# Kernel optimization log

Hardware: AMD Instinct MI355X
Metric: run time of the kernel (lower is better)

## Reference

```python
import jax, jax.numpy as jnp
import numpy as np

C = 60                 # channels
WINDOW_SIZES = [4, 8, 12]
SHIFTS = 4
BN_EPS = 1e-5


def setup_inputs() -> dict:
    key = jax.random.key(0)
    ks = jax.random.split(key, 4)
    s = 0.05
    return {
        "x": jax.random.normal(ks[0], (8, C, 288, 288), dtype=jnp.float32),
        # project_inp: Conv2d(C, 2C, k=1) + BatchNorm2d(2C) (inference form)
        "W_in": jax.random.normal(ks[1], (2 * C, C), dtype=jnp.float32) * s,
        "b_in": jnp.zeros((2 * C,), dtype=jnp.float32),
        "bn_gamma": jnp.ones((2 * C,), dtype=jnp.float32),
        "bn_beta": jnp.zeros((2 * C,), dtype=jnp.float32),
        "bn_mean": jax.random.normal(ks[2], (2 * C,), dtype=jnp.float32) * s,
        "bn_var": jnp.ones((2 * C,), dtype=jnp.float32),
        # project_out: Conv2d(C, C, k=1)
        "W_out": jax.random.normal(ks[3], (C, C), dtype=jnp.float32) * s,
        "b_out": jnp.zeros((C,), dtype=jnp.float32),
    }


def _window_self_attn(x_, wsize, shift):
    """One GMSA branch: roll -> window partition -> QQ^T softmax V -> merge -> unroll.
    x_ : [b, 2c, H, W] where first c channels are q, last c are v."""
    b, c2, H, W = x_.shape
    c = c2 // 2
    if shift > 0:
        x_ = jnp.roll(x_, shift=(-(wsize // 2), -(wsize // 2)), axis=(2, 3))
    nh, nw = H // wsize, W // wsize
    # 'b (qv c) (h dh) (w dw) -> qv (b h w) (dh dw) c'
    xw = x_.reshape(b, 2, c, nh, wsize, nw, wsize)
    xw = xw.transpose(1, 0, 3, 5, 4, 6, 2).reshape(2, b * nh * nw, wsize * wsize, c)
    q, v = xw[0], xw[1]                      # [n, p, c] with p = wsize*wsize
    atn = jax.nn.softmax(jnp.einsum("npc,nqc->npq", q, q), axis=-1)
    y = jnp.einsum("npq,nqc->npc", atn, v)
    # '(b h w) (dh dw) c -> b c (h dh) (w dw)'
    y = y.reshape(b, nh, nw, wsize, wsize, c).transpose(0, 5, 1, 3, 2, 4)
    y = y.reshape(b, c, H, W)
    if shift > 0:
        y = jnp.roll(y, shift=(wsize // 2, wsize // 2), axis=(2, 3))
    return y, atn


def reference(x, W_in, b_in, bn_gamma, bn_beta, bn_mean, bn_var, W_out, b_out):
    # 1x1 conv = channel matmul, then inference BatchNorm
    xp = jnp.einsum("oc,bchw->bohw", W_in, x) + b_in[None, :, None, None]
    inv = bn_gamma / jnp.sqrt(bn_var + BN_EPS)
    xp = xp * inv[None, :, None, None] + (bn_beta - bn_mean * inv)[None, :, None, None]
    split = 2 * C // 3  # = 40 per branch (q,v interleaved as 2x20)
    ys, atns = [], []
    off = 0
    for ws in WINDOW_SIZES:
        y_, a_ = _window_self_attn(xp[:, off:off + split], ws, SHIFTS)
        off += split
        ys.append(y_)
        atns.append(a_)
    y = jnp.concatenate(ys, axis=1)  # [b, C, H, W]
    y = jnp.einsum("oc,bchw->bohw", W_out, y) + b_out[None, :, None, None]
    return (y, atns[0], atns[1], atns[2])
```

## Files before the change

### kernel.cpp

```cpp
#include <hip/hip_runtime.h>


constexpr int HW = 288 * 288;
constexpr long long ATN0_OFF = 39813120LL;
constexpr long long ATN1_OFF = ATN0_OFF + 41472LL * 256;
constexpr long long ATN2_OFF = ATN1_OFF + 10368LL * 4096;

constexpr size_t YB_OFF = 0;
constexpr size_t WP_OFF = 79626240;
constexpr size_t BP_OFF = WP_OFF + 28800;
constexpr size_t XP_OFF = BP_OFF + 512;

typedef __attribute__((ext_vector_type(8))) short     bf16x8;
typedef __attribute__((ext_vector_type(4))) short     bf16x4;
typedef __attribute__((ext_vector_type(4))) float     f32x4;
typedef __attribute__((ext_vector_type(4))) unsigned  u32x4;
typedef __attribute__((ext_vector_type(2))) unsigned  u32x2;

__device__ __forceinline__ unsigned bfrnd(float f) {
    unsigned u = __float_as_uint(f);
    return (u + 0x7fffu + ((u >> 16) & 1u)) >> 16;
}
__device__ __forceinline__ unsigned bfpack(float a, float b) { return bfrnd(a) | (bfrnd(b) << 16); }

#if defined(__has_builtin)
#if __has_builtin(__builtin_amdgcn_mfma_f32_16x16x16bf16_1k)
#define HAVE_MFMA16 1
#endif
#endif

__device__ __forceinline__ f32x4 mfma16(bf16x4 a, bf16x4 b, f32x4 c) {
#ifdef HAVE_MFMA16
    return __builtin_amdgcn_mfma_f32_16x16x16bf16_1k(a, b, c, 0, 0, 0);
#else
    f32x4 d;
    asm("v_mfma_f32_16x16x16_bf16 %0, %1, %2, %3" : "=v"(d) : "v"(a), "v"(b), "v"(c));
    return d;
#endif
}

__device__ __forceinline__ f32x4 mfma32(bf16x8 a, bf16x8 b, f32x4 c) {
    return __builtin_amdgcn_mfma_f32_16x16x32_bf16(a, b, c, 0, 0, 0);
}

__global__ void prep_kernel(const float* __restrict__ W_in, const float* __restrict__ b_in,
                            const float* __restrict__ gamma, const float* __restrict__ beta,
                            const float* __restrict__ mean, const float* __restrict__ var,
                            float* __restrict__ Wp, float* __restrict__ bp) {
    int o = threadIdx.x;
    if (o < 120) {
        float inv = gamma[o] / sqrtf(var[o] + 1e-5f);
        for (int c = 0; c < 60; ++c) Wp[o * 60 + c] = W_in[o * 60 + c] * inv;
        bp[o] = b_in[o] * inv + beta[o] - mean[o] * inv;
    } else if (o < 128) {
        bp[o] = 0.f;
    }
}

__global__ __launch_bounds__(256, 3) void proj_in_kernel(const float* __restrict__ x,
                                                         const float* __restrict__ Wp,
                                                         const float* __restrict__ bp,
                                                         unsigned short* __restrict__ xp) {
    __shared__ __align__(16) unsigned short wq[128 * 64];
    __shared__ __align__(16) unsigned short ys[128 * 120];

    const int tid = threadIdx.x;
    const long long pixel0 = (long long)blockIdx.x * 128;
    const int b   = (int)(pixel0 / HW);
    const int hw0 = (int)(pixel0 % HW);

    for (int i = tid; i < 8192; i += 256) {
        const int row = i >> 6, ch = i & 63;
        wq[i] = (row < 120 && ch < 60) ? (unsigned short)bfrnd(Wp[row * 60 + ch]) : (unsigned short)0;
    }

    const int wave = tid >> 6, lane = tid & 63, lo = lane & 15, g = lane >> 4;

    u32x4 xlo[2], xhi[2];
    #pragma unroll
    for (int mt2 = 0; mt2 < 2; ++mt2) {
        const int row = (wave * 2 + mt2) * 16 + lo;
        const float* xb = x + (long long)b * 60 * HW + hw0 + row;
        unsigned short tl[8], th[8];
        #pragma unroll
        for (int e = 0; e < 8; ++e) {
            const int cl = g * 8 + e;
            tl[e] = (unsigned short)bfrnd(xb[(long long)cl * HW]);
            const int ch = 32 + g * 8 + e;
            th[e] = (ch < 60) ? (unsigned short)bfrnd(xb[(long long)ch * HW]) : (unsigned short)0;
        }
        xlo[mt2] = *reinterpret_cast<const u32x4*>(tl);
        xhi[mt2] = *reinterpret_cast<const u32x4*>(th);
    }
    __syncthreads();

    #pragma unroll
    for (int n = 0; n < 8; ++n) {
        u32x4 wfl = *reinterpret_cast<const u32x4*>(&wq[(n * 16 + lo) * 64 + g * 8]);
        u32x4 wfh = *reinterpret_cast<const u32x4*>(&wq[(n * 16 + lo) * 64 + 32 + g * 8]);
        const int oc0 = n * 16 + 4 * g;
        const f32x4 bpv = *reinterpret_cast<const f32x4*>(&bp[oc0]);
        #pragma unroll
        for (int mt2 = 0; mt2 < 2; ++mt2) {
            f32x4 z = {0.f, 0.f, 0.f, 0.f};
            f32x4 acc = mfma32(*reinterpret_cast<bf16x8*>(&wfl),
                               *reinterpret_cast<bf16x8*>(&xlo[mt2]), z);
            acc = mfma32(*reinterpret_cast<bf16x8*>(&wfh),
                         *reinterpret_cast<bf16x8*>(&xhi[mt2]), acc);
            if (oc0 < 120) {
                const int pixel = (wave * 2 + mt2) * 16 + lo;
                u32x2 t;
                t.x = bfpack(acc[0] + bpv[0], acc[1] + bpv[1]);
                t.y = bfpack(acc[2] + bpv[2], acc[3] + bpv[3]);
                *reinterpret_cast<u32x2*>(&ys[pixel * 120 + oc0]) = t;
            }
        }
    }
    __syncthreads();

    for (int i = tid; i < 3 * 1280; i += 256) {
        const int br = i / 1280, j = i - br * 1280, p = j / 10, c = j - p * 10;
        const u32x2 v = *reinterpret_cast<const u32x2*>(&ys[p * 120 + br * 40 + c * 4]);
        reinterpret_cast<u32x2*>(xp + ((long long)(b * 3 + br) * HW + hw0) * 40)[p * 10 + c] = v;
    }
}

template <int WS, int NWIN, int BLOCK, int WPW, int BRANCH, int MINW>
__launch_bounds__(BLOCK, MINW)
__global__ void branch_kernel(const unsigned short* __restrict__ xp,
                              unsigned short* __restrict__ ybuf,
                              float* __restrict__ atn) {
    constexpr int P    = WS * WS;
    constexpr int RT   = P / 16;
    constexpr int SH   = WS / 2;
    constexpr int NWND = 288 / WS;
    constexpr int RSTR = 56;
    constexpr int WAVES = BLOCK / 64;
    constexpr int WINS_PER_WAVE = (NWIN * WPW) / WAVES;

    __shared__ __align__(16) unsigned short qv[NWIN * P * RSTR];
    __shared__ __align__(16) unsigned short ys[NWIN * P * 20];

    const int tid = threadIdx.x;
    const int w0 = blockIdx.x * NWIN;

    for (int idx = tid; idx < NWIN * P * 5; idx += BLOCK) {
        const int wl  = idx / (P * 5);
        const int rem = idx - wl * (P * 5);
        const int pix = rem / 5;
        const int ck  = rem - pix * 5;
        const int w   = w0 + wl;
        const int b   = w / (NWND * NWND);
        const int r2  = w - b * (NWND * NWND);
        const int wi  = r2 / NWND;
        const int wj  = r2 - wi * NWND;
        const int gh  = (wi * WS + pix / WS + SH) % 288;
        const int gw  = (wj * WS + pix % WS + SH) % 288;
        const u32x4 d = *reinterpret_cast<const u32x4*>(
            xp + ((long long)(b * 3 + BRANCH) * HW + gh * 288 + gw) * 40 + ck * 8);
        *reinterpret_cast<u32x4*>(&qv[(wl * P + pix) * RSTR + ck * 8]) = d;
    }
    __syncthreads();

    const int wave = tid >> 6;
    const int lane = tid & 63;
    const int lo   = lane & 15;
    const int g    = lane >> 4;

    for (int wk = 0; wk < WINS_PER_WAVE; ++wk) {
        const int wl   = (WPW == 1) ? (wave * WINS_PER_WAVE + wk) : (wave >> 1);
        const int half = (WPW == 1) ? 0 : (wave & 1);
        const int w    = w0 + wl;
        const unsigned short* wbase = qv + wl * P * RSTR;

        bf16x8 F[RT];
        #pragma unroll
        for (int t = 0; t < RT; ++t) {
            u32x4 u = *reinterpret_cast<const u32x4*>(&wbase[(16 * t + lo) * RSTR + g * 8]);
            if (g == 2) { u.z = 0; u.w = 0; }
            if (g == 3) { u.x = 0; u.y = 0; u.z = 0; u.w = 0; }
            F[t] = *reinterpret_cast<bf16x8*>(&u);
        }

        bf16x4 VB[RT][2];
        #pragma unroll
        for (int i = 0; i < RT; ++i) {
            #pragma unroll
            for (int ct = 0; ct < 2; ++ct) {
                const int c = ct * 16 + lo;
                bf16x4 vv;
                #pragma unroll
                for (int jj = 0; jj < 4; ++jj) {
                    const int row = 16 * i + 4 * g + jj;
                    vv[jj] = (c < 20) ? (short)wbase[row * RSTR + 20 + c] : (short)0;
                }
                VB[i][ct] = vv;
            }
        }

        const int jstart = (WPW == 1) ? 0 : (half * ((RT + 1) / 2));
        const int jend   = (WPW == 1) ? RT : ((half == 0) ? ((RT + 1) / 2) : RT);
        for (int j = jstart; j < jend; ++j) {
            f32x4 S[RT];
            #pragma unroll
            for (int i = 0; i < RT; ++i) {
                f32x4 z = {0.f, 0.f, 0.f, 0.f};
                S[i] = mfma32(F[i], F[j], z);
            }

            float m0 = S[0][0], m1 = S[0][1], m2 = S[0][2], m3 = S[0][3];
            #pragma unroll
            for (int i = 1; i < RT; ++i) {
                m0 = fmaxf(m0, S[i][0]); m1 = fmaxf(m1, S[i][1]);
                m2 = fmaxf(m2, S[i][2]); m3 = fmaxf(m3, S[i][3]);
            }
            float m = fmaxf(fmaxf(m0, m1), fmaxf(m2, m3));
            m = fmaxf(m, __shfl_xor(m, 16));
            m = fmaxf(m, __shfl_xor(m, 32));

            float s0 = 0.f, s1 = 0.f, s2 = 0.f, s3 = 0.f;
            #pragma unroll
            for (int i = 0; i < RT; ++i) {
                float e0 = __expf(S[i][0] - m); S[i][0] = e0; s0 += e0;
                float e1 = __expf(S[i][1] - m); S[i][1] = e1; s1 += e1;
                float e2 = __expf(S[i][2] - m); S[i][2] = e2; s2 += e2;
                float e3 = __expf(S[i][3] - m); S[i][3] = e3; s3 += e3;
            }
            float sum = (s0 + s1) + (s2 + s3);
            sum += __shfl_xor(sum, 16);
            sum += __shfl_xor(sum, 32);
            const float inv = 1.0f / sum;
            #pragma unroll
            for (int i = 0; i < RT; ++i) {
                S[i][0] *= inv; S[i][1] *= inv; S[i][2] *= inv; S[i][3] *= inv;
            }

            float* arow = atn + ((long long)w * P + 16 * j + lo) * P + 4 * g;
            #pragma unroll
            for (int i = 0; i < RT; ++i)
                __builtin_nontemporal_store(S[i], reinterpret_cast<f32x4*>(arow + 16 * i));

            f32x4 Y0 = {0.f, 0.f, 0.f, 0.f};
            f32x4 Y1 = {0.f, 0.f, 0.f, 0.f};
            #pragma unroll
            for (int i = 0; i < RT; ++i) {
                u32x2 t2;
                t2.x = bfpack(S[i][0], S[i][1]);
                t2.y = bfpack(S[i][2], S[i][3]);
                bf16x4 pa = *reinterpret_cast<bf16x4*>(&t2);
                Y0 = mfma16(pa, VB[i][0], Y0);
                Y1 = mfma16(pa, VB[i][1], Y1);
            }

            unsigned short* ywp = ys + (wl * P + 16 * j + 4 * g) * 20;
            #pragma unroll
            for (int r = 0; r < 4; ++r) ywp[r * 20 + lo] = (unsigned short)bfrnd(Y0[r]);
            if (lo < 4) {
                #pragma unroll
                for (int r = 0; r < 4; ++r) ywp[r * 20 + 16 + lo] = (unsigned short)bfrnd(Y1[r]);
            }
        }
    }
    __syncthreads();

    for (int i = tid; i < NWIN * P * 5; i += BLOCK) {
        const int wl   = i / (P * 5);
        const int rem  = i - wl * (P * 5);
        const int pixr = rem / 5;
        const int c    = rem - pixr * 5;
        const int w2   = w0 + wl;
        const int b2   = w2 / (NWND * NWND);
        const int r2   = w2 - b2 * (NWND * NWND);
        const int wi2  = r2 / NWND;
        const int wj2  = r2 - wi2 * NWND;
        const int oh   = (wi2 * WS + pixr / WS + SH) % 288;
        const int ow   = (wj2 * WS + pixr % WS + SH) % 288;
        const u32x2 v = *reinterpret_cast<const u32x2*>(&ys[(wl * P + pixr) * 20 + c * 4]);
        *reinterpret_cast<u32x2*>(
            ybuf + ((long long)(b2 * 3 + BRANCH) * HW + oh * 288 + ow) * 20 + c * 4) = v;
    }
}

__global__ __launch_bounds__(256, 4) void proj_out_kernel(const unsigned short* __restrict__ ybuf,
                                                          const float* __restrict__ W_out,
                                                          const float* __restrict__ bout,
                                                          float* __restrict__ out) {
    __shared__ __align__(16) unsigned short yh[128 * 72];
    __shared__ __align__(16) unsigned short wq[64 * 64];

    const int tid = threadIdx.x;
    const long long pixel0 = (long long)blockIdx.x * 128;
    const int b   = (int)(pixel0 / HW);
    const int hw0 = (int)(pixel0 % HW);

    for (int i = tid; i < 4096; i += 256) {
        const int row = i >> 6, ch = i & 63;
        wq[i] = (row < 60 && ch < 60) ? (unsigned short)bfrnd(W_out[row * 60 + ch]) : (unsigned short)0;
    }

    for (int i = tid; i < 1920; i += 256) {
        const int br = i / 640, j = i - br * 640, p = j / 5, c = j - p * 5;
        const u32x2 v = reinterpret_cast<const u32x2*>(
            ybuf + ((long long)(b * 3 + br) * HW + hw0) * 20)[j];
        *reinterpret_cast<u32x2*>(&yh[p * 72 + br * 20 + c * 4]) = v;
    }
    {
        const int p = tid >> 1, hh = tid & 1;
        u32x2 zz; zz.x = 0; zz.y = 0;
        *reinterpret_cast<u32x2*>(&yh[p * 72 + 60 + hh * 4]) = zz;
    }
    __syncthreads();

    const int wave = tid >> 6, lane = tid & 63, lo = lane & 15, g = lane >> 4;

    u32x4 alo[2], ahi[2];
    #pragma unroll
    for (int mt2 = 0; mt2 < 2; ++mt2) {
        const int row = (wave * 2 + mt2) * 16 + lo;
        alo[mt2] = *reinterpret_cast<const u32x4*>(&yh[row * 72 + g * 8]);
        ahi[mt2] = *reinterpret_cast<const u32x4*>(&yh[row * 72 + 32 + g * 8]);
    }

    #pragma unroll
    for (int n = 0; n < 4; ++n) {
        u32x4 wfl = *reinterpret_cast<const u32x4*>(&wq[(n * 16 + lo) * 64 + g * 8]);
        u32x4 wfh = *reinterpret_cast<const u32x4*>(&wq[(n * 16 + lo) * 64 + 32 + g * 8]);
        const int oc = n * 16 + lo;
        const float bo = (oc < 60) ? bout[oc] : 0.f;
        #pragma unroll
        for (int mt2 = 0; mt2 < 2; ++mt2) {
            f32x4 z = {0.f, 0.f, 0.f, 0.f};
            f32x4 acc = mfma32(*reinterpret_cast<bf16x8*>(&alo[mt2]),
                               *reinterpret_cast<bf16x8*>(&wfl), z);
            acc = mfma32(*reinterpret_cast<bf16x8*>(&ahi[mt2]),
                         *reinterpret_cast<bf16x8*>(&wfh), acc);
            if (oc < 60) {
                const int px = (wave * 2 + mt2) * 16 + 4 * g;
                f32x4 v;
                v[0] = acc[0] + bo; v[1] = acc[1] + bo;
                v[2] = acc[2] + bo; v[3] = acc[3] + bo;
                __builtin_nontemporal_store(v, reinterpret_cast<f32x4*>(
                    &out[((long long)b * 60 + oc) * HW + hw0 + px]));
            }
        }
    }
}

extern "C" void kernel_launch(void* const* d_in, const int* in_sizes, int n_in,
                              void* d_out, int out_size, void* d_ws, size_t ws_size,
                              hipStream_t stream) {
    const float* x     = (const float*)d_in[0];
    const float* W_in  = (const float*)d_in[1];
    const float* b_in  = (const float*)d_in[2];
    const float* gamma = (const float*)d_in[3];
    const float* beta  = (const float*)d_in[4];
    const float* mean  = (const float*)d_in[5];
    const float* var   = (const float*)d_in[6];
    const float* Wout  = (const float*)d_in[7];
    const float* bout  = (const float*)d_in[8];
    float* out = (float*)d_out;

    char* wsb = (char*)d_ws;
    unsigned short* ybuf = (unsigned short*)(wsb + YB_OFF);
    float*          Wp   = (float*)(wsb + WP_OFF);
    float*          bp   = (float*)(wsb + BP_OFF);
    unsigned short* xp   = (unsigned short*)(wsb + XP_OFF);

    prep_kernel<<<1, 128, 0, stream>>>(W_in, b_in, gamma, beta, mean, var, Wp, bp);
    proj_in_kernel<<<5184, 256, 0, stream>>>(x, Wp, bp, xp);

    branch_kernel<4,  8, 128, 1, 0, 4><<<5184, 128, 0, stream>>>(xp, ybuf, out + ATN0_OFF);
    branch_kernel<8,  2, 128, 1, 1, 4><<<5184, 128, 0, stream>>>(xp, ybuf, out + ATN1_OFF);
    branch_kernel<12, 1, 128, 2, 2, 3><<<4608, 128, 0, stream>>>(xp, ybuf, out + ATN2_OFF);

    proj_out_kernel<<<5184, 256, 0, stream>>>(ybuf, Wout, bout, out);
}
```

Baseline: 441.0 us.

## Merge three window-attention branch kernels into one interleaved launch

Replaces the three separate per-branch attention launches with a single kernel whose blocks dispatch to one of three templated bodies by block index, interleaving branches round-robin and giving the leftover branch-0/1 blocks the tail. Shared memory is unified into one buffer sized for the largest branch. The goal is to remove launch gaps and tail effects between the branch kernels and let branches with different costs overlap on the GPU. In exchange, all branches now share one register/launch-bounds setting (min 3 waves per EU) and the larger shared allocation, which may reduce occupancy for the small-window branches.

Result: slower. 452.5 us (+2.6%).

```diff
diff --git a/kernel.cpp b/kernel.cpp
--- a/kernel.cpp
+++ b/kernel.cpp
@@ -125,11 +125,11 @@
     }
 }
 
-template <int WS, int NWIN, int BLOCK, int WPW, int BRANCH, int MINW>
-__launch_bounds__(BLOCK, MINW)
-__global__ void branch_kernel(const unsigned short* __restrict__ xp,
-                              unsigned short* __restrict__ ybuf,
-                              float* __restrict__ atn) {
+template <int WS, int NWIN, int BLOCK, int WPW, int BRANCH>
+__device__ __forceinline__ void branch_body(char* smem,
+                                            const unsigned short* __restrict__ xp,
+                                            unsigned short* __restrict__ ybuf,
+                                            float* __restrict__ atn, int blk) {
     constexpr int P    = WS * WS;
     constexpr int RT   = P / 16;
     constexpr int SH   = WS / 2;
@@ -138,11 +138,11 @@
     constexpr int WAVES = BLOCK / 64;
     constexpr int WINS_PER_WAVE = (NWIN * WPW) / WAVES;
 
-    __shared__ __align__(16) unsigned short qv[NWIN * P * RSTR];
-    __shared__ __align__(16) unsigned short ys[NWIN * P * 20];
+    unsigned short* qv = reinterpret_cast<unsigned short*>(smem);
+    unsigned short* ys = reinterpret_cast<unsigned short*>(smem) + NWIN * P * RSTR;
 
     const int tid = threadIdx.x;
-    const int w0 = blockIdx.x * NWIN;
+    const int w0 = blk * NWIN;
 
     for (int idx = tid; idx < NWIN * P * 5; idx += BLOCK) {
         const int wl  = idx / (P * 5);
@@ -281,6 +281,22 @@
     }
 }
 
+__global__ __launch_bounds__(128, 3) void branches_kernel(const unsigned short* __restrict__ xp,
+                                                          unsigned short* __restrict__ ybuf,
+                                                          float* __restrict__ atn0,
+                                                          float* __restrict__ atn1,
+                                                          float* __restrict__ atn2) {
+    __shared__ __align__(16) char smem[21888];
+    const int bid = blockIdx.x;
+    int branch, blk;
+    if (bid < 13824) { branch = bid % 3;            blk = bid / 3; }
+    else             { int t = bid - 13824; branch = t & 1; blk = 4608 + (t >> 1); }
+
+    if (branch == 0)      branch_body<4,  8, 128, 1, 0>(smem, xp, ybuf, atn0, blk);
+    else if (branch == 1) branch_body<8,  2, 128, 1, 1>(smem, xp, ybuf, atn1, blk);
+    else                  branch_body<12, 1, 128, 2, 2>(smem, xp, ybuf, atn2, blk);
+}
+
 __global__ __launch_bounds__(256, 4) void proj_out_kernel(const unsigned short* __restrict__ ybuf,
                                                           const float* __restrict__ W_out,
                                                           const float* __restrict__ bout,
@@ -368,10 +384,7 @@
 
     prep_kernel<<<1, 128, 0, stream>>>(W_in, b_in, gamma, beta, mean, var, Wp, bp);
     proj_in_kernel<<<5184, 256, 0, stream>>>(x, Wp, bp, xp);
-
-    branch_kernel<4,  8, 128, 1, 0, 4><<<5184, 128, 0, stream>>>(xp, ybuf, out + ATN0_OFF);
-    branch_kernel<8,  2, 128, 1, 1, 4><<<5184, 128, 0, stream>>>(xp, ybuf, out + ATN1_OFF);
-    branch_kernel<12, 1, 128, 2, 2, 3><<<4608, 128, 0, stream>>>(xp, ybuf, out + ATN2_OFF);
-
+    branches_kernel<<<14976, 128, 0, stream>>>(xp, ybuf,
+                                               out + ATN0_OFF, out + ATN1_OFF, out + ATN2_OFF);
     proj_out_kernel<<<5184, 256, 0, stream>>>(ybuf, Wout, bout, out);
 }
```
